# Optimization experiments

Measured on AMD Instinct MI355X. Metric: run time of the kernel, lower is better.

Reference implementation:

```python
import jax, jax.numpy as jnp
import numpy as np

D_IN = 64   # per-branch feature dim ('input' in module)
D_OUT = 32  # final output dim
N = 16384   # number of nodes (cells)


def setup_inputs() -> dict:
    key = jax.random.key(0)
    ks = jax.random.split(key, 8)
    z = jax.random.normal(ks[0], (N, 2 * D_IN), dtype=jnp.float32)
    adj = jax.random.uniform(ks[1], (N, N), dtype=jnp.float32)
    s = 1.0 / np.sqrt(D_IN)
    # GCLayer weights: y = adj @ (x @ W) + b, stored [in, out]
    W0 = jax.random.uniform(ks[2], (D_IN, D_IN), jnp.float32, -s, s)
    b0 = jax.random.uniform(ks[3], (D_IN,), jnp.float32, -s, s)
    W1 = jax.random.uniform(ks[4], (D_IN, D_IN), jnp.float32, -s, s)
    b1 = jax.random.uniform(ks[5], (D_IN,), jnp.float32, -s, s)
    sl = 1.0 / np.sqrt(2 * D_IN)
    # final nn.Linear(2*input, output): torch layout [out, in]
    Wl = jax.random.uniform(ks[6], (D_OUT, 2 * D_IN), jnp.float32, -sl, sl)
    bl = jax.random.uniform(ks[7], (D_OUT,), jnp.float32, -sl, sl)
    return {"z": z, "adj": adj, "W0": W0, "b0": b0, "W1": W1, "b1": b1,
            "Wl": Wl, "bl": bl}


def reference(z, adj, W0, b0, W1, b1, Wl, bl):
    elu = jax.nn.elu

    def gc(x, W, b):
        # GCLayer: adjacency aggregation of linearly transformed features
        return adj @ (x @ W) + b

    zs, zu = z[:, :D_IN], z[:, D_IN:]
    # layer 0 (shared weights across both branches, as in the torch code)
    ys = elu(gc(elu(zs), W0, b0))
    yu = elu(gc(elu(zu), W0, b0))
    # layer 1
    ys = elu(gc(ys, W1, b1))
    yu = elu(gc(yu, W1, b1))
    y = jnp.concatenate((ys, yu), axis=-1)
    return y @ Wl.T + bl
```

## Files before the change

### kernel.cpp

```cpp
#include <hip/hip_runtime.h>
#include <hip/hip_bf16.h>


#define NN 16384
#define C2 128
#define DIN 64
#define DOUT 32

typedef __attribute__((ext_vector_type(8))) __bf16 bf16x8;
typedef __attribute__((ext_vector_type(4))) float f32x4;

__device__ __forceinline__ float eluf(float x) {
    return x > 0.f ? x : __expf(x) - 1.f;
}

__device__ __forceinline__ unsigned short f2bf(float f) {
    unsigned u = __float_as_uint(f);
    u += 0x7FFFu + ((u >> 16) & 1u);
    return (unsigned short)(u >> 16);
}

template <bool ELU_IN>
__global__ __launch_bounds__(256)
void small_mm(const float* __restrict__ X, const float* __restrict__ W,
              unsigned short* __restrict__ Tcm)
{
    __shared__ float WsT[DIN * DIN];
    const int tid = threadIdx.x;
    for (int i = tid; i < DIN * DIN; i += 256) {
        int c = i >> 6, k = i & 63;
        WsT[i] = W[k * DIN + c];
    }
    __syncthreads();

    const int r     = tid & 63;
    const int chalf = (tid >> 6) & 1;
    const int cq    = tid >> 7;
    const size_t row = (size_t)blockIdx.x * 64 + r;

    float e[DIN];
    const float* xp = X + row * C2 + chalf * DIN;
#pragma unroll
    for (int i = 0; i < 16; i++) {
        float4 v = ((const float4*)xp)[i];
        if (ELU_IN) { v.x = eluf(v.x); v.y = eluf(v.y); v.z = eluf(v.z); v.w = eluf(v.w); }
        e[i*4+0] = v.x; e[i*4+1] = v.y; e[i*4+2] = v.z; e[i*4+3] = v.w;
    }

    for (int j = 0; j < 32; j++) {
        int cc = cq * 32 + j;
        const float* wr = WsT + cc * DIN;
        float a = 0.f;
#pragma unroll
        for (int k = 0; k < DIN; k += 4) {
            float4 w = *(const float4*)(wr + k);
            a += e[k]*w.x + e[k+1]*w.y + e[k+2]*w.z + e[k+3]*w.w;
        }
        int c = (chalf << 6) + cc;
        Tcm[(size_t)c * NN + row] = f2bf(a);
    }
}

__global__ __launch_bounds__(256, 2)
void big_gemm(const float* __restrict__ A, const unsigned short* __restrict__ Bcm,
              const float* __restrict__ bias, float* __restrict__ Y)
{
    __shared__ unsigned short As[32 * 136];
    __shared__ unsigned short Bs[128 * 136];

    const int tid  = threadIdx.x;
    const int lane = tid & 63;
    const int wave = tid >> 6;
    const int m    = lane & 15;
    const int kq   = lane >> 4;
    const size_t row0 = (size_t)blockIdx.x * 32;

    f32x4 acc[2][2];
#pragma unroll
    for (int i = 0; i < 2; i++)
#pragma unroll
        for (int j = 0; j < 2; j++) acc[i][j] = (f32x4){0.f, 0.f, 0.f, 0.f};

    for (int k0 = 0; k0 < NN; k0 += 128) {
        __syncthreads();
#pragma unroll
        for (int i = 0; i < 4; i++) {
            int id = tid + i * 256;
            int r  = id >> 5;
            int kk = (id & 31) * 4;
            float4 v = *(const float4*)(A + (row0 + r) * (size_t)NN + k0 + kk);
            unsigned lo = f2bf(v.x) | ((unsigned)f2bf(v.y) << 16);
            unsigned hi = f2bf(v.z) | ((unsigned)f2bf(v.w) << 16);
            *(uint2*)(&As[r * 136 + kk]) = make_uint2(lo, hi);
        }
#pragma unroll
        for (int i = 0; i < 8; i++) {
            int id = tid + i * 256;
            int c  = id >> 4;
            int kk = (id & 15) * 8;
            float4 v = *(const float4*)(Bcm + (size_t)c * NN + k0 + kk);
            *(float4*)(&Bs[c * 136 + kk]) = v;
        }
        __syncthreads();
#pragma unroll
        for (int s = 0; s < 4; s++) {
            bf16x8 a0 = *(const bf16x8*)(&As[ m       * 136 + s * 32 + kq * 8]);
            bf16x8 a1 = *(const bf16x8*)(&As[(16 + m) * 136 + s * 32 + kq * 8]);
            bf16x8 b0 = *(const bf16x8*)(&Bs[(wave * 32 + m     ) * 136 + s * 32 + kq * 8]);
            bf16x8 b1 = *(const bf16x8*)(&Bs[(wave * 32 + 16 + m) * 136 + s * 32 + kq * 8]);
            acc[0][0] = __builtin_amdgcn_mfma_f32_16x16x32_bf16(a0, b0, acc[0][0], 0, 0, 0);
            acc[1][0] = __builtin_amdgcn_mfma_f32_16x16x32_bf16(a1, b0, acc[1][0], 0, 0, 0);
            acc[0][1] = __builtin_amdgcn_mfma_f32_16x16x32_bf16(a0, b1, acc[0][1], 0, 0, 0);
            acc[1][1] = __builtin_amdgcn_mfma_f32_16x16x32_bf16(a1, b1, acc[1][1], 0, 0, 0);
        }
    }

#pragma unroll
    for (int mt = 0; mt < 2; mt++)
#pragma unroll
        for (int nt = 0; nt < 2; nt++) {
            int cc = wave * 32 + nt * 16 + m;
            float b = bias[cc & 63];
#pragma unroll
            for (int reg = 0; reg < 4; reg++) {
                size_t rr = row0 + mt * 16 + kq * 4 + reg;
                float v = acc[mt][nt][reg] + b;
                v = v > 0.f ? v : __expf(v) - 1.f;
                Y[rr * C2 + cc] = v;
            }
        }
}

__global__ __launch_bounds__(256)
void final_mm(const float* __restrict__ Y, const float* __restrict__ Wl,
              const float* __restrict__ bl, float* __restrict__ out)
{
    __shared__ float WlT[C2 * DOUT];
    __shared__ float red[4 * 64 * 33];
    const int tid = threadIdx.x;
    for (int i = tid; i < C2 * DOUT; i += 256) {
        int c = i >> 5, o = i & 31;
        WlT[i] = Wl[o * C2 + c];
    }
    __syncthreads();

    const int r  = tid & 63;
    const int cq = tid >> 6;
    const size_t row = (size_t)blockIdx.x * 64 + r;

    float acc[DOUT];
#pragma unroll
    for (int o = 0; o < DOUT; o++) acc[o] = 0.f;

    const float* yp = Y + row * C2 + cq * 32;
#pragma unroll
    for (int i = 0; i < 8; i++) {
        float4 y = ((const float4*)yp)[i];
        int cb = cq * 32 + i * 4;
#pragma unroll
        for (int o4 = 0; o4 < 8; o4++) {
            float4 w0 = *(const float4*)(WlT + (cb + 0) * DOUT + o4 * 4);
            float4 w1 = *(const float4*)(WlT + (cb + 1) * DOUT + o4 * 4);
            float4 w2 = *(const float4*)(WlT + (cb + 2) * DOUT + o4 * 4);
            float4 w3 = *(const float4*)(WlT + (cb + 3) * DOUT + o4 * 4);
            acc[o4*4+0] += y.x*w0.x + y.y*w1.x + y.z*w2.x + y.w*w3.x;
            acc[o4*4+1] += y.x*w0.y + y.y*w1.y + y.z*w2.y + y.w*w3.y;
            acc[o4*4+2] += y.x*w0.z + y.y*w1.z + y.z*w2.z + y.w*w3.z;
            acc[o4*4+3] += y.x*w0.w + y.y*w1.w + y.z*w2.w + y.w*w3.w;
        }
    }

    float* myred = red + (cq * 64 + r) * 33;
#pragma unroll
    for (int o = 0; o < DOUT; o++) myred[o] = acc[o];
    __syncthreads();

#pragma unroll
    for (int j = 0; j < 8; j++) {
        int id = tid + 256 * j;
        int o  = id & 31;
        int rr = id >> 5;
        float s = bl[o] + red[(0 * 64 + rr) * 33 + o] + red[(1 * 64 + rr) * 33 + o]
                        + red[(2 * 64 + rr) * 33 + o] + red[(3 * 64 + rr) * 33 + o];
        out[((size_t)blockIdx.x * 64 + rr) * DOUT + o] = s;
    }
}

extern "C" void kernel_launch(void* const* d_in, const int* in_sizes, int n_in,
                              void* d_out, int out_size, void* d_ws, size_t ws_size,
                              hipStream_t stream)
{
    const float* z   = (const float*)d_in[0];
    const float* adj = (const float*)d_in[1];
    const float* W0  = (const float*)d_in[2];
    const float* b0  = (const float*)d_in[3];
    const float* W1  = (const float*)d_in[4];
    const float* b1  = (const float*)d_in[5];
    const float* Wl  = (const float*)d_in[6];
    const float* bl  = (const float*)d_in[7];
    float* out = (float*)d_out;

    unsigned short* T = (unsigned short*)d_ws;
    float* Y = (float*)((char*)d_ws + (size_t)C2 * NN * sizeof(unsigned short));

    small_mm<true ><<<NN / 64, 256, 0, stream>>>(z, W0, T);
    big_gemm      <<<NN / 32, 256, 0, stream>>>(adj, T, b0, Y);
    small_mm<false><<<NN / 64, 256, 0, stream>>>(Y, W1, T);
    big_gemm      <<<NN / 32, 256, 0, stream>>>(adj, T, b1, Y);
    final_mm      <<<NN / 64, 256, 0, stream>>>(Y, Wl, bl, out);
}
```

Measured before the change: 1.702 ms.

## Split-K big GEMM with register-direct MFMA loads and fused bias/ELU downstream

The adjacency GEMM now splits K into two halves across paired blocks, so 1024 blocks run instead of 512. It drops LDS staging: each wave loads A (fp32, converted to bf16 in registers) and B fragments straight from global memory with a two-stage register double buffer. The partial sums are written to two buffers, and the following small_mm and final_mm kernels add them, apply the bias and ELU. This aims to raise parallelism and occupancy and remove LDS and barrier overhead. The cost is an extra partial-result buffer in memory traffic and uncoalesced per-lane global loads.

Measured after the change: 2.655 ms. +56.0%, slower.

```diff
diff --git a/kernel.cpp b/kernel.cpp
--- a/kernel.cpp
+++ b/kernel.cpp
@@ -6,6 +6,7 @@
 #define C2 128
 #define DIN 64
 #define DOUT 32
+#define KHALF 8192
 
 typedef __attribute__((ext_vector_type(8))) __bf16 bf16x8;
 typedef __attribute__((ext_vector_type(4))) float f32x4;
@@ -20,9 +21,10 @@
     return (unsigned short)(u >> 16);
 }
 
-template <bool ELU_IN>
+template <bool ELU_IN, bool PARTIAL>
 __global__ __launch_bounds__(256)
-void small_mm(const float* __restrict__ X, const float* __restrict__ W,
+void small_mm(const float* __restrict__ X, const float* __restrict__ X2,
+              const float* __restrict__ bias, const float* __restrict__ W,
               unsigned short* __restrict__ Tcm)
 {
     __shared__ float WsT[DIN * DIN];
@@ -39,11 +41,21 @@
     const size_t row = (size_t)blockIdx.x * 64 + r;
 
     float e[DIN];
-    const float* xp = X + row * C2 + chalf * DIN;
+    const float* xp  = X + row * C2 + chalf * DIN;
+    const float* xp2 = PARTIAL ? (X2 + row * C2 + chalf * DIN) : xp;
 #pragma unroll
     for (int i = 0; i < 16; i++) {
         float4 v = ((const float4*)xp)[i];
-        if (ELU_IN) { v.x = eluf(v.x); v.y = eluf(v.y); v.z = eluf(v.z); v.w = eluf(v.w); }
+        if (PARTIAL) {
+            float4 v2 = ((const float4*)xp2)[i];
+            float4 bv = ((const float4*)bias)[i];
+            v.x = eluf(v.x + v2.x + bv.x);
+            v.y = eluf(v.y + v2.y + bv.y);
+            v.z = eluf(v.z + v2.z + bv.z);
+            v.w = eluf(v.w + v2.w + bv.w);
+        } else if (ELU_IN) {
+            v.x = eluf(v.x); v.y = eluf(v.y); v.z = eluf(v.z); v.w = eluf(v.w);
+        }
         e[i*4+0] = v.x; e[i*4+1] = v.y; e[i*4+2] = v.z; e[i*4+3] = v.w;
     }
 
@@ -61,78 +73,83 @@
     }
 }
 
-__global__ __launch_bounds__(256, 2)
+struct StepRegs { float4 a0, a1; bf16x8 b0, b1, b2, b3; };
+
+__global__ __launch_bounds__(256, 4)
 void big_gemm(const float* __restrict__ A, const unsigned short* __restrict__ Bcm,
-              const float* __restrict__ bias, float* __restrict__ Y)
-{
-    __shared__ unsigned short As[32 * 136];
-    __shared__ unsigned short Bs[128 * 136];
-
+              float* __restrict__ Yp)
+{
+    const int bid  = blockIdx.x;
+    const int kh   = bid & 1;
+    const int rb   = bid >> 1;
     const int tid  = threadIdx.x;
     const int lane = tid & 63;
-    const int wave = tid >> 6;
+    const int w    = tid >> 6;
+    const int rowg = w & 1;
+    const int colg = w >> 1;
     const int m    = lane & 15;
     const int kq   = lane >> 4;
-    const size_t row0 = (size_t)blockIdx.x * 32;
-
-    f32x4 acc[2][2];
-#pragma unroll
-    for (int i = 0; i < 2; i++)
-#pragma unroll
-        for (int j = 0; j < 2; j++) acc[i][j] = (f32x4){0.f, 0.f, 0.f, 0.f};
-
-    for (int k0 = 0; k0 < NN; k0 += 128) {
-        __syncthreads();
-#pragma unroll
-        for (int i = 0; i < 4; i++) {
-            int id = tid + i * 256;
-            int r  = id >> 5;
-            int kk = (id & 31) * 4;
-            float4 v = *(const float4*)(A + (row0 + r) * (size_t)NN + k0 + kk);
-            unsigned lo = f2bf(v.x) | ((unsigned)f2bf(v.y) << 16);
-            unsigned hi = f2bf(v.z) | ((unsigned)f2bf(v.w) << 16);
-            *(uint2*)(&As[r * 136 + kk]) = make_uint2(lo, hi);
-        }
-#pragma unroll
-        for (int i = 0; i < 8; i++) {
-            int id = tid + i * 256;
-            int c  = id >> 4;
-            int kk = (id & 15) * 8;
-            float4 v = *(const float4*)(Bcm + (size_t)c * NN + k0 + kk);
-            *(float4*)(&Bs[c * 136 + kk]) = v;
-        }
-        __syncthreads();
-#pragma unroll
-        for (int s = 0; s < 4; s++) {
-            bf16x8 a0 = *(const bf16x8*)(&As[ m       * 136 + s * 32 + kq * 8]);
-            bf16x8 a1 = *(const bf16x8*)(&As[(16 + m) * 136 + s * 32 + kq * 8]);
-            bf16x8 b0 = *(const bf16x8*)(&Bs[(wave * 32 + m     ) * 136 + s * 32 + kq * 8]);
-            bf16x8 b1 = *(const bf16x8*)(&Bs[(wave * 32 + 16 + m) * 136 + s * 32 + kq * 8]);
-            acc[0][0] = __builtin_amdgcn_mfma_f32_16x16x32_bf16(a0, b0, acc[0][0], 0, 0, 0);
-            acc[1][0] = __builtin_amdgcn_mfma_f32_16x16x32_bf16(a1, b0, acc[1][0], 0, 0, 0);
-            acc[0][1] = __builtin_amdgcn_mfma_f32_16x16x32_bf16(a0, b1, acc[0][1], 0, 0, 0);
-            acc[1][1] = __builtin_amdgcn_mfma_f32_16x16x32_bf16(a1, b1, acc[1][1], 0, 0, 0);
-        }
-    }
-
-#pragma unroll
-    for (int mt = 0; mt < 2; mt++)
-#pragma unroll
-        for (int nt = 0; nt < 2; nt++) {
-            int cc = wave * 32 + nt * 16 + m;
-            float b = bias[cc & 63];
-#pragma unroll
-            for (int reg = 0; reg < 4; reg++) {
-                size_t rr = row0 + mt * 16 + kq * 4 + reg;
-                float v = acc[mt][nt][reg] + b;
-                v = v > 0.f ? v : __expf(v) - 1.f;
-                Y[rr * C2 + cc] = v;
-            }
-        }
+
+    const size_t kbase = (size_t)kh * KHALF;
+    const float* Ap = A + (size_t)(rb * 32 + rowg * 16 + m) * NN + kbase + kq * 8;
+    const unsigned short* Bp0 = Bcm + (size_t)(colg * 64 + m) * NN + kbase + kq * 8;
+    const unsigned short* Bp1 = Bp0 + (size_t)16 * NN;
+    const unsigned short* Bp2 = Bp0 + (size_t)32 * NN;
+    const unsigned short* Bp3 = Bp0 + (size_t)48 * NN;
+
+    f32x4 acc0 = {0.f,0.f,0.f,0.f}, acc1 = {0.f,0.f,0.f,0.f};
+    f32x4 acc2 = {0.f,0.f,0.f,0.f}, acc3 = {0.f,0.f,0.f,0.f};
+
+    auto load = [&](StepRegs& s, int k) {
+        s.a0 = *(const float4*)(Ap + k);
+        s.a1 = *(const float4*)(Ap + k + 4);
+        s.b0 = *(const bf16x8*)(Bp0 + k);
+        s.b1 = *(const bf16x8*)(Bp1 + k);
+        s.b2 = *(const bf16x8*)(Bp2 + k);
+        s.b3 = *(const bf16x8*)(Bp3 + k);
+    };
+    auto comp = [&](const StepRegs& s) {
+        bf16x8 af;
+        af[0] = (__bf16)s.a0.x; af[1] = (__bf16)s.a0.y;
+        af[2] = (__bf16)s.a0.z; af[3] = (__bf16)s.a0.w;
+        af[4] = (__bf16)s.a1.x; af[5] = (__bf16)s.a1.y;
+        af[6] = (__bf16)s.a1.z; af[7] = (__bf16)s.a1.w;
+        acc0 = __builtin_amdgcn_mfma_f32_16x16x32_bf16(af, s.b0, acc0, 0, 0, 0);
+        acc1 = __builtin_amdgcn_mfma_f32_16x16x32_bf16(af, s.b1, acc1, 0, 0, 0);
+        acc2 = __builtin_amdgcn_mfma_f32_16x16x32_bf16(af, s.b2, acc2, 0, 0, 0);
+        acc3 = __builtin_amdgcn_mfma_f32_16x16x32_bf16(af, s.b3, acc3, 0, 0, 0);
+    };
+
+    StepRegs sA, sB;
+    load(sA, 0);
+    int k = 0;
+    for (int t = 0; t < 127; ++t) {
+        load(sB, k + 32);
+        comp(sA);
+        load(sA, k + 64);
+        comp(sB);
+        k += 64;
+    }
+    load(sB, k + 32);
+    comp(sA);
+    comp(sB);
+
+    float* Yw = Yp + (size_t)kh * NN * C2;
+    const int row0 = rb * 32 + rowg * 16 + kq * 4;
+    const int col0 = colg * 64 + m;
+#pragma unroll
+    for (int reg = 0; reg < 4; ++reg) {
+        float* yr = Yw + (size_t)(row0 + reg) * C2 + col0;
+        yr[0]  = acc0[reg];
+        yr[16] = acc1[reg];
+        yr[32] = acc2[reg];
+        yr[48] = acc3[reg];
+    }
 }
 
 __global__ __launch_bounds__(256)
-void final_mm(const float* __restrict__ Y, const float* __restrict__ Wl,
+void final_mm(const float* __restrict__ P0, const float* __restrict__ P1,
+              const float* __restrict__ b1, const float* __restrict__ Wl,
               const float* __restrict__ bl, float* __restrict__ out)
 {
     __shared__ float WlT[C2 * DOUT];
@@ -152,10 +169,18 @@
 #pragma unroll
     for (int o = 0; o < DOUT; o++) acc[o] = 0.f;
 
-    const float* yp = Y + row * C2 + cq * 32;
+    const float* yp  = P0 + row * C2 + cq * 32;
+    const float* yp2 = P1 + row * C2 + cq * 32;
+    const float* bq  = b1 + (cq & 1) * 32;
 #pragma unroll
     for (int i = 0; i < 8; i++) {
-        float4 y = ((const float4*)yp)[i];
+        float4 y  = ((const float4*)yp)[i];
+        float4 y2 = ((const float4*)yp2)[i];
+        float4 bv = *(const float4*)(bq + i * 4);
+        y.x = eluf(y.x + y2.x + bv.x);
+        y.y = eluf(y.y + y2.y + bv.y);
+        y.z = eluf(y.z + y2.z + bv.z);
+        y.w = eluf(y.w + y2.w + bv.w);
         int cb = cq * 32 + i * 4;
 #pragma unroll
         for (int o4 = 0; o4 < 8; o4++) {
@@ -201,11 +226,13 @@
     float* out = (float*)d_out;
 
     unsigned short* T = (unsigned short*)d_ws;
-    float* Y = (float*)((char*)d_ws + (size_t)C2 * NN * sizeof(unsigned short));
-
-    small_mm<true ><<<NN / 64, 256, 0, stream>>>(z, W0, T);
-    big_gemm      <<<NN / 32, 256, 0, stream>>>(adj, T, b0, Y);
-    small_mm<false><<<NN / 64, 256, 0, stream>>>(Y, W1, T);
-    big_gemm      <<<NN / 32, 256, 0, stream>>>(adj, T, b1, Y);
-    final_mm      <<<NN / 64, 256, 0, stream>>>(Y, Wl, bl, out);
-}
+    float* Yp  = (float*)((char*)d_ws + (size_t)C2 * NN * sizeof(unsigned short));
+    float* Yp0 = Yp;
+    float* Yp1 = Yp + (size_t)NN * C2;
+
+    small_mm<true,  false><<<NN / 64, 256, 0, stream>>>(z, nullptr, nullptr, W0, T);
+    big_gemm             <<<1024,     256, 0, stream>>>(adj, T, Yp);
+    small_mm<false, true ><<<NN / 64, 256, 0, stream>>>(Yp0, Yp1, b0, W1, T);
+    big_gemm             <<<1024,     256, 0, stream>>>(adj, T, Yp);
+    final_mm             <<<NN / 64, 256, 0, stream>>>(Yp0, Yp1, b1, Wl, bl, out);
+}
```
